# Kernel optimization log

Hardware: AMD Instinct MI355X
Metric: run time of the kernel (lower is better)

## Reference

```python
import jax, jax.numpy as jnp
import numpy as np
from math import sqrt

NUM_HEADS = 16
NUM_KV_HEADS = 4
ROPE_BASE = 10000.0


def setup_inputs() -> dict:
    key = jax.random.key(0)
    ks = jax.random.split(key, 9)
    B, S, E = 4, 2048, 2048
    KV_DIM = NUM_KV_HEADS * (E // NUM_HEADS)  # 512
    s = 0.02
    return {
        "x": jax.random.normal(ks[0], (B, S, E), jnp.float32),
        "wq": jax.random.normal(ks[1], (E, E), jnp.float32) * s,
        "bq": jnp.zeros((E,), jnp.float32),
        "wk": jax.random.normal(ks[2], (KV_DIM, E), jnp.float32) * s,
        "bk": jnp.zeros((KV_DIM,), jnp.float32),
        "wv": jax.random.normal(ks[3], (KV_DIM, E), jnp.float32) * s,
        "bv": jnp.zeros((KV_DIM,), jnp.float32),
        "wo": jax.random.normal(ks[4], (E, E), jnp.float32) * s,
        "bo": jnp.zeros((E,), jnp.float32),
    }


def _rope_cos_sin(seq_len, head_dim, dtype):
    inv_freq = 1.0 / (ROPE_BASE ** (jnp.arange(0, head_dim, 2, dtype=jnp.float32) / head_dim))
    pos = jnp.arange(seq_len, dtype=jnp.float32)
    freqs = pos[:, None] * inv_freq[None, :]            # [S, D/2]
    emb = jnp.concatenate([freqs, freqs], axis=-1)      # [S, D]
    return jnp.cos(emb).astype(dtype), jnp.sin(emb).astype(dtype)


def _apply_rope(t, cos, sin):
    # t: [B, H, S, D]; cos/sin: [S, D]
    d2 = t.shape[-1] // 2
    rot = jnp.concatenate([-t[..., d2:], t[..., :d2]], axis=-1)
    return t * cos[None, None, :, :] + rot * sin[None, None, :, :]


def reference(x, wq, bq, wk, bk, wv, bv, wo, bo):
    B, S, E = x.shape
    H, KV = NUM_HEADS, NUM_KV_HEADS
    D = E // H
    G = H // KV

    q = (x @ wq.T + bq).reshape(B, S, H, D).transpose(0, 2, 1, 3)   # [B,H,S,D]
    k = (x @ wk.T + bk).reshape(B, S, KV, D).transpose(0, 2, 1, 3)  # [B,KV,S,D]
    v = (x @ wv.T + bv).reshape(B, S, KV, D).transpose(0, 2, 1, 3)

    cos, sin = _rope_cos_sin(S, D, x.dtype)
    q = _apply_rope(q, cos, sin)
    k = _apply_rope(k, cos, sin)

    # GQA: expand each kv head group_size times (contiguous repeat)
    k = jnp.repeat(k, G, axis=1)  # [B,H,S,D]
    v = jnp.repeat(v, G, axis=1)

    scores = jnp.einsum("bhqd,bhkd->bhqk", q, k)
    causal = jnp.triu(jnp.ones((S, S), dtype=bool), k=1)
    scores = jnp.where(causal[None, None, :, :], -jnp.inf, scores)
    attn = jax.nn.softmax(scores / sqrt(D), axis=-1)
    out = jnp.einsum("bhqk,bhkd->bhqd", attn, v)        # [B,H,S,D]
    out = out.transpose(0, 2, 1, 3).reshape(B, S, E)
    return out @ wo.T + bo
```

## Files before the change

kernel.cpp:

```cpp
#include <hip/hip_runtime.h>
#include <stdint.h>
#include <math.h>

typedef __attribute__((ext_vector_type(8))) short s16x8;
typedef __attribute__((ext_vector_type(4))) short s16x4;
typedef __attribute__((ext_vector_type(4))) float f32x4;

#define NEGH (-1.0e30f)

__device__ __forceinline__ short f2bf(float f) {
  union { float f; unsigned int i; } c; c.f = f;
  unsigned int lsb = (c.i >> 16) & 1u;
  c.i += 0x7fffu + lsb;
  return (short)(c.i >> 16);
}
__device__ __forceinline__ float bf2f(short u) {
  union { unsigned int i; float f; } c;
  c.i = ((unsigned int)(unsigned short)u) << 16;
  return c.f;
}

#define GLOAD_LDS16(gp, lp)                                                  \
  __builtin_amdgcn_global_load_lds(                                          \
      (__attribute__((address_space(1))) void*)(void*)(gp),                  \
      (__attribute__((address_space(3))) void*)(lp), 16, 0, 0)

__global__ __launch_bounds__(256) void cvt_kernel(const float* __restrict__ in,
                                                  short* __restrict__ out)
{
  const size_t i = ((size_t)blockIdx.x * 256 + threadIdx.x) * 4;
  const float4 v = *(const float4*)(in + i);
  s16x4 o = { f2bf(v.x), f2bf(v.y), f2bf(v.z), f2bf(v.w) };
  *(s16x4*)(out + i) = o;
}

__global__ __launch_bounds__(256) void gemm_bt(
    const short* __restrict__ A, const short* __restrict__ W,
    const float* __restrict__ bias, const float* __restrict__ bias2,
    void* __restrict__ C, void* __restrict__ C2,
    int M, int N, int K, int omode)
{
  __shared__ __align__(16) short As[128 * 64];
  __shared__ __align__(16) short Bs[128 * 64];

  const int t = threadIdx.x;
  const int l = t & 63;
  const int w = t >> 6;
  const int lane16 = l & 15;
  const int quad = l >> 4;
  const int wm = w >> 1, wn = w & 1;

  int bx = blockIdx.x, by = blockIdx.y;
  if (gridDim.x == 8 && gridDim.y == 64) {
    const int lid = blockIdx.x + 8 * blockIdx.y;
    const int xcd = lid & 7, idx = lid >> 3;
    by = xcd * 8 + (idx >> 3);
    bx = idx & 7;
  }
  const int mb0 = by * 128;
  const int nb0 = bx * 128;

  const f32x4 zero = {0.f, 0.f, 0.f, 0.f};
  f32x4 acc[4][4];
#pragma unroll
  for (int i = 0; i < 4; ++i)
#pragma unroll
    for (int j = 0; j < 4; ++j) acc[i][j] = zero;

  const int sr = t >> 3;
  const int sp = t & 7;
  const short* Ag = A + (size_t)(mb0 + sr) * K + sp * 8;
  const short* Wg = W + (size_t)(nb0 + sr) * K + sp * 8;
  short* Al = As + t * 8;
  short* Bl = Bs + t * 8;

  const int nkt = K >> 6;
  for (int kt = 0; kt < nkt; ++kt) {
    __syncthreads();
    const int kof = kt * 64;
#pragma unroll
    for (int it = 0; it < 4; ++it) {
      GLOAD_LDS16(Ag + kof + (size_t)(it * 32) * K, Al + it * 2048);
      GLOAD_LDS16(Wg + kof + (size_t)(it * 32) * K, Bl + it * 2048);
    }
    __syncthreads();
#pragma unroll
    for (int kk = 0; kk < 2; ++kk) {
      s16x8 af[4], bf[4];
#pragma unroll
      for (int mi = 0; mi < 4; ++mi)
        af[mi] = *(const s16x8*)&As[(wm * 64 + mi * 16 + lane16) * 64 +
                                    kk * 32 + quad * 8];
#pragma unroll
      for (int ni = 0; ni < 4; ++ni)
        bf[ni] = *(const s16x8*)&Bs[(wn * 64 + ni * 16 + lane16) * 64 +
                                    kk * 32 + quad * 8];
#pragma unroll
      for (int mi = 0; mi < 4; ++mi)
#pragma unroll
        for (int ni = 0; ni < 4; ++ni)
          acc[mi][ni] = __builtin_amdgcn_mfma_f32_16x16x32_bf16(
              af[mi], bf[ni], acc[mi][ni], 0, 0, 0);
    }
  }

#pragma unroll
  for (int ni = 0; ni < 4; ++ni) {
    const int n = nb0 + wn * 64 + ni * 16 + lane16;
    const float bvx = (omode == 3 && n >= 512) ? bias2[n - 512] : bias[n];
#pragma unroll
    for (int mi = 0; mi < 4; ++mi) {
      const int m0 = mb0 + wm * 64 + mi * 16 + quad * 4;
#pragma unroll
      for (int r = 0; r < 4; ++r) {
        const int m = m0 + r;
        const float v = acc[mi][ni][r] + bvx;
        if (omode == 0) {
          ((short*)C)[(size_t)m * N + n] = f2bf(v);
        } else if (omode == 1) {
          ((float*)C)[(size_t)m * N + n] = v;
        } else {
          if (n < 512) ((short*)C)[(size_t)m * 512 + n] = f2bf(v);
          else         ((short*)C2)[(size_t)m * 512 + (n - 512)] = f2bf(v);
        }
      }
    }
  }
}

__global__ __launch_bounds__(512, 2) void gemm256_bt(
    const short* __restrict__ A, const short* __restrict__ W,
    const float* __restrict__ bias, void* __restrict__ C,
    int M, int N, int K, int omode)
{
  __shared__ __align__(16) short Asm[2 * 16384];
  __shared__ __align__(16) short Bsm[2 * 16384];

  const int t = threadIdx.x;
  const int l = t & 63;
  const int w = t >> 6;
  const int lane16 = l & 15;
  const int quad = l >> 4;
  const int wm = w >> 2;
  const int wn = w & 3;

  int bx = blockIdx.x, by = blockIdx.y;
  if (gridDim.x == 8 && gridDim.y == 32) {
    const int bid = blockIdx.y * 8 + blockIdx.x;
    const int xcd = bid & 7, idx = bid >> 3;
    const int xc = xcd & 3, yc = xcd >> 2;
    bx = xc * 2 + (idx & 1);
    by = yc * 16 + (idx >> 1);
  }
  const int mb0 = by * 256;
  const int nb0 = bx * 256;

  const f32x4 zero = {0.f, 0.f, 0.f, 0.f};
  f32x4 acc[8][4];
#pragma unroll
  for (int i = 0; i < 8; ++i)
#pragma unroll
    for (int j = 0; j < 4; ++j) acc[i][j] = zero;

  const int srow = t >> 2;
  const int scs = (t & 3) ^ ((t >> 3) & 3);
  const short* Ag = A + (size_t)(mb0 + srow) * K + scs * 8;
  const short* Wg = W + (size_t)(nb0 + srow) * K + scs * 8;
  const size_t rstep = (size_t)128 * K;

#define STAGE_A(b, kt, kh)                                                    \
  do {                                                                        \
    const size_t ko_ = (size_t)(kt) * 64 + (kh) * 32;                         \
    GLOAD_LDS16(Ag + ko_,         Asm + (b) * 16384 + (kh) * 8192 + t * 8);   \
    GLOAD_LDS16(Ag + ko_ + rstep, Asm + (b) * 16384 + (kh) * 8192 + 4096 + t * 8); \
  } while (0)
#define STAGE_B(b, kt, kh)                                                    \
  do {                                                                        \
    const size_t ko_ = (size_t)(kt) * 64 + (kh) * 32;                         \
    GLOAD_LDS16(Wg + ko_,         Bsm + (b) * 16384 + (kh) * 8192 + t * 8);   \
    GLOAD_LDS16(Wg + ko_ + rstep, Bsm + (b) * 16384 + (kh) * 8192 + 4096 + t * 8); \
  } while (0)

  s16x8 bfr[4];

#define DO_PHASE(BUF, KK, MG, READB, STAGE_STMT, DO_VM)                       \
  {                                                                           \
    const short* Abase = Asm + (BUF) * 16384 + (KK) * 8192;                   \
    const short* Bbase = Bsm + (BUF) * 16384 + (KK) * 8192;                   \
    if (READB) {                                                              \
      _Pragma("unroll")                                                       \
      for (int ni = 0; ni < 4; ++ni) {                                        \
        const int nr = wn * 64 + ni * 16 + lane16;                            \
        bfr[ni] = *(const s16x8*)(Bbase + nr * 32 +                           \
                                  ((quad ^ ((nr >> 1) & 3)) << 3));           \
      }                                                                       \
    }                                                                         \
    s16x8 afr[4];                                                             \
    _Pragma("unroll")                                                         \
    for (int mi2 = 0; mi2 < 4; ++mi2) {                                       \
      const int mr = wm * 128 + (MG) * 64 + mi2 * 16 + lane16;                \
      afr[mi2] = *(const s16x8*)(Abase + mr * 32 +                            \
                                 ((quad ^ ((mr >> 1) & 3)) << 3));            \
    }                                                                         \
    STAGE_STMT;                                                               \
    __builtin_amdgcn_s_barrier();                                             \
    asm volatile("s_waitcnt lgkmcnt(0)" ::: "memory");                        \
    __builtin_amdgcn_sched_barrier(0);                                        \
    __builtin_amdgcn_s_setprio(1);                                            \
    _Pragma("unroll")                                                         \
    for (int mi2 = 0; mi2 < 4; ++mi2)                                         \
      _Pragma("unroll")                                                       \
      for (int ni = 0; ni < 4; ++ni)                                          \
        acc[(MG) * 4 + mi2][ni] = __builtin_amdgcn_mfma_f32_16x16x32_bf16(    \
            afr[mi2], bfr[ni], acc[(MG) * 4 + mi2][ni], 0, 0, 0);             \
    __builtin_amdgcn_s_setprio(0);                                            \
    if (DO_VM) {                                                              \
      asm volatile("s_waitcnt vmcnt(10)" ::: "memory");                       \
      __builtin_amdgcn_sched_barrier(0);                                      \
    }                                                                         \
    __builtin_amdgcn_s_barrier();                                             \
  }

  const int NT = K >> 6;

  STAGE_B(0, 0, 0); STAGE_A(0, 0, 0); STAGE_B(0, 0, 1); STAGE_A(0, 0, 1);
  STAGE_B(1, 1, 0); STAGE_A(1, 1, 0); STAGE_B(1, 1, 1);
  asm volatile("s_waitcnt vmcnt(10)" ::: "memory");
  __builtin_amdgcn_sched_barrier(0);
  __builtin_amdgcn_s_barrier();

  for (int i2 = 0; i2 < NT; i2 += 2) {
    const int tp1 = (i2 + 1 < NT) ? i2 + 1 : NT - 1;
    const int tp2 = (i2 + 2 < NT) ? i2 + 2 : NT - 1;
    const int tp3 = (i2 + 3 < NT) ? i2 + 3 : NT - 1;
    DO_PHASE(0, 0, 0, true,  STAGE_A(1, tp1, 1), false)
    DO_PHASE(0, 0, 1, false, STAGE_B(0, tp2, 0), true)
    DO_PHASE(0, 1, 0, true,  STAGE_A(0, tp2, 0), false)
    DO_PHASE(0, 1, 1, false, STAGE_B(0, tp2, 1), true)
    DO_PHASE(1, 0, 0, true,  STAGE_A(0, tp2, 1), false)
    DO_PHASE(1, 0, 1, false, STAGE_B(1, tp3, 0), true)
    DO_PHASE(1, 1, 0, true,  STAGE_A(1, tp3, 0), false)
    DO_PHASE(1, 1, 1, false, STAGE_B(1, tp3, 1), true)
  }

#pragma unroll
  for (int ni = 0; ni < 4; ++ni) {
    const int n = nb0 + wn * 64 + ni * 16 + lane16;
    const float bv = bias[n];
#pragma unroll
    for (int mi = 0; mi < 8; ++mi) {
      const int m0 = mb0 + wm * 128 + mi * 16 + quad * 4;
#pragma unroll
      for (int r = 0; r < 4; ++r) {
        const float v = acc[mi][ni][r] + bv;
        if (omode == 0) ((short*)C)[(size_t)(m0 + r) * N + n] = f2bf(v);
        else            ((float*)C)[(size_t)(m0 + r) * N + n] = v;
      }
    }
  }
#undef DO_PHASE
#undef STAGE_A
#undef STAGE_B
}

__global__ __launch_bounds__(256) void rope_tab_kernel(float2* __restrict__ tab)
{
  const int i = blockIdx.x * 256 + threadIdx.x;
  const int pos = i >> 6, d = i & 63;
  const float fr = (float)pos * exp2f((float)d * -0.20762050593048584f);
  float sn, cs;
  sincosf(fr, &sn, &cs);
  tab[i] = make_float2(cs, sn);
}

__global__ __launch_bounds__(256) void rope_kernel(short* __restrict__ buf,
                                                   int lognh,
                                                   const float2* __restrict__ tab)
{
  const int idx = blockIdx.x * 256 + threadIdx.x;
  const int d = idx & 63;
  const int rest = idx >> 6;
  const int row = rest >> lognh;
  const int pos = row & 2047;
  const float2 cssn = tab[(pos << 6) | d];
  const float cs = cssn.x, sn = cssn.y;
  const size_t base = (size_t)rest * 128 + d;
  const float lo = bf2f(buf[base]);
  const float hi = bf2f(buf[base + 64]);
  buf[base]      = f2bf(lo * cs - hi * sn);
  buf[base + 64] = f2bf(hi * cs + lo * sn);
}

__global__ __launch_bounds__(256) void trans_kernel(const short* __restrict__ in,
                                                    short* __restrict__ out)
{
  __shared__ short T[64 * 72];
  const int t = threadIdx.x;
  const int ms = blockIdx.x * 64;
  const int ns = blockIdx.y * 64;
  const int b = ms >> 11;
  const int sl = ms & 2047;
  const int r = t >> 3, sg = t & 7;
#pragma unroll
  for (int j = 0; j < 2; ++j) {
    const uint4 v = *(const uint4*)(in + (size_t)(ms + r + 32 * j) * 512 + ns + sg * 8);
    *(uint4*)&T[(r + 32 * j) * 72 + sg * 8] = v;
  }
  __syncthreads();
#pragma unroll
  for (int j = 0; j < 2; ++j) {
    const int nr = r + 32 * j;
    s16x8 v;
#pragma unroll
    for (int i = 0; i < 8; ++i) v[i] = T[(sg * 8 + i) * 72 + nr];
    *(s16x8*)(out + ((size_t)(b * 512 + ns + nr)) * 2048 + sl + sg * 8) = v;
  }
}

__global__ __launch_bounds__(512, 4) void attn_kernel(
    const short* __restrict__ qg, const short* __restrict__ kg,
    const short* __restrict__ vtg, short* __restrict__ og)
{
  __shared__ __align__(16) short Ksm[64 * 128];
  __shared__ __align__(16) short Vsm[128 * 64];
  __shared__ __align__(16) short Psm[128 * 64];

  const int t = threadIdx.x;
  const int l = t & 63;
  const int w = t >> 6;
  const int lane16 = l & 15;
  const int quad = l >> 4;

  const int lid = blockIdx.x + 8 * (blockIdx.y + 16 * blockIdx.z);
  const int xcd = lid & 7, idx = lid >> 3;
  const int g = xcd * 2 + (idx >> 5);
  const int wv_ = idx & 31;
  const int b = g >> 2, kv = g & 3;
  const int h = kv * 4 + (wv_ >> 3);
  const int jb = wv_ & 7;

  const int krow = t >> 4, kseg = t & 15;
  const int vrow = t >> 3, vseg = t & 7;
  const int kswz = (kseg ^ (krow & 7)) * 8;
  const int vswz = (vseg ^ (vrow & 7)) * 8;

  const short* kbaseptr = kg + ((size_t)(b * 2048)) * 512 + kv * 128;
  const short* vbaseptr = vtg + ((size_t)(b * 512 + kv * 128)) * 2048;

  const float SC = 0.08838834764831845f * 1.4426950408889634f;
  const f32x4 zero = {0.f, 0.f, 0.f, 0.f};
  const int swz = (lane16 & 7) << 3;

  uint4 kr0, kr1, vr0, vr1;
#define LOADT(KB)                                                             \
  do {                                                                        \
    kr0 = *(const uint4*)(kbaseptr + (size_t)((KB) + krow) * 512 + kseg * 8); \
    kr1 = *(const uint4*)(kbaseptr + (size_t)((KB) + 32 + krow) * 512 + kseg * 8); \
    vr0 = *(const uint4*)(vbaseptr + (size_t)(vrow) * 2048 + (KB) + vseg * 8);     \
    vr1 = *(const uint4*)(vbaseptr + (size_t)(64 + vrow) * 2048 + (KB) + vseg * 8);\
  } while (0)
#define WRITET()                                                              \
  do {                                                                        \
    *(uint4*)&Ksm[krow * 128 + kswz] = kr0;                                   \
    *(uint4*)&Ksm[(32 + krow) * 128 + kswz] = kr1;                            \
    *(uint4*)&Vsm[vrow * 64 + vswz] = vr0;                                    \
    *(uint4*)&Vsm[(64 + vrow) * 64 + vswz] = vr1;                             \
  } while (0)

  for (int sp2 = 0; sp2 < 2; ++sp2) {
    const int jj = sp2 ? (15 - jb) : jb;
    const int qb0 = jj * 128;
    const int qw0 = qb0 + w * 16;
    const int qmaxw = qw0 + 15;
    const int ntl = 2 * jj + 2;

    s16x8 qf[4];
    {
      const short* qrow =
          qg + ((size_t)(b * 2048 + qw0 + lane16)) * 2048 + h * 128 + quad * 8;
#pragma unroll
      for (int kk = 0; kk < 4; ++kk) qf[kk] = *(const s16x8*)(qrow + kk * 32);
    }

    f32x4 o[8];
#pragma unroll
    for (int i = 0; i < 8; ++i) o[i] = zero;
    float m_i = NEGH, l_i = 0.f;

    LOADT(0);
    WRITET();

    for (int tl = 0; tl < ntl; ++tl) {
      __syncthreads();
      const int kbase = tl * 64;
      if (tl + 1 < ntl) LOADT((tl + 1) * 64);

      if (kbase <= qmaxw) {
        f32x4 st[4];
#pragma unroll
        for (int mt = 0; mt < 4; ++mt) st[mt] = zero;
        __builtin_amdgcn_s_setprio(1);
#pragma unroll
        for (int mt = 0; mt < 4; ++mt) {
          const int rb = (mt * 16 + lane16) * 128;
#pragma unroll
          for (int kk = 0; kk < 4; ++kk) {
            const s16x8 a = *(const s16x8*)&Ksm[rb + ((kk * 32 + quad * 8) ^ swz)];
            st[mt] = __builtin_amdgcn_mfma_f32_16x16x32_bf16(a, qf[kk], st[mt], 0, 0, 0);
          }
        }
        __builtin_amdgcn_s_setprio(0);

        const bool maskt = (kbase + 63 > qw0);
        const int qabs = qw0 + lane16;
        float tl_ = NEGH;
        if (maskt) {
#pragma unroll
          for (int mt = 0; mt < 4; ++mt)
#pragma unroll
            for (int r = 0; r < 4; ++r) {
              float xx = st[mt][r];
              if ((kbase + mt * 16 + quad * 4 + r) > qabs) xx = NEGH;
              st[mt][r] = xx;
              tl_ = fmaxf(tl_, xx);
            }
        } else {
#pragma unroll
          for (int mt = 0; mt < 4; ++mt)
#pragma unroll
            for (int r = 0; r < 4; ++r) tl_ = fmaxf(tl_, st[mt][r]);
        }
        tl_ = fmaxf(tl_, __shfl_xor(tl_, 16));
        tl_ = fmaxf(tl_, __shfl_xor(tl_, 32));
        const float mnew = fmaxf(m_i, tl_);
        if (!__all(tl_ <= m_i)) {
          const float alpha = exp2f((m_i - mnew) * SC);
          l_i *= alpha;
#pragma unroll
          for (int r = 0; r < 4; ++r) {
            const float ar = __shfl(alpha, quad * 4 + r);
#pragma unroll
            for (int ntd = 0; ntd < 8; ++ntd) o[ntd][r] *= ar;
          }
        }
        m_i = mnew;
        const float mS = mnew * SC;
        float rs = 0.f;
#pragma unroll
        for (int mt = 0; mt < 4; ++mt) {
          const float p0 = exp2f(fmaf(st[mt][0], SC, -mS));
          const float p1 = exp2f(fmaf(st[mt][1], SC, -mS));
          const float p2 = exp2f(fmaf(st[mt][2], SC, -mS));
          const float p3 = exp2f(fmaf(st[mt][3], SC, -mS));
          rs += (p0 + p1) + (p2 + p3);
          uint2 pk2;
          asm("v_cvt_pk_bf16_f32 %0, %1, %2" : "=v"(pk2.x) : "v"(p0), "v"(p1));
          asm("v_cvt_pk_bf16_f32 %0, %1, %2" : "=v"(pk2.y) : "v"(p2), "v"(p3));
          *(uint2*)&Psm[(w * 16 + lane16) * 64 + ((mt * 16 + quad * 4) ^ swz)] = pk2;
        }
        rs += __shfl_xor(rs, 16);
        rs += __shfl_xor(rs, 32);
        l_i += rs;

        const int prb = (w * 16 + lane16) * 64;
        __builtin_amdgcn_s_setprio(1);
#pragma unroll
        for (int kk = 0; kk < 2; ++kk) {
          const s16x8 pf = *(const s16x8*)&Psm[prb + ((kk * 32 + quad * 8) ^ swz)];
#pragma unroll
          for (int ntd = 0; ntd < 8; ++ntd) {
            const s16x8 vf =
                *(const s16x8*)&Vsm[(ntd * 16 + lane16) * 64 + ((kk * 32 + quad * 8) ^ swz)];
            o[ntd] = __builtin_amdgcn_mfma_f32_16x16x32_bf16(pf, vf, o[ntd], 0, 0, 0);
          }
        }
        __builtin_amdgcn_s_setprio(0);
      }

      __syncthreads();
      if (tl + 1 < ntl) WRITET();
    }

#pragma unroll
    for (int r = 0; r < 4; ++r) {
      const float lr = __shfl(l_i, quad * 4 + r);
      const float inv = 1.f / lr;
      const size_t base =
          ((size_t)(b * 2048 + qw0 + quad * 4 + r)) * 2048 + h * 128 + lane16;
#pragma unroll
      for (int ntd = 0; ntd < 8; ++ntd) og[base + ntd * 16] = f2bf(o[ntd][r] * inv);
    }
  }
#undef LOADT
#undef WRITET
}

extern "C" void kernel_launch(void* const* d_in, const int* in_sizes, int n_in,
                              void* d_out, int out_size, void* d_ws,
                              size_t ws_size, hipStream_t stream)
{
  const float* x  = (const float*)d_in[0];
  const float* wq = (const float*)d_in[1];
  const float* bq = (const float*)d_in[2];
  const float* wk = (const float*)d_in[3];
  const float* bk = (const float*)d_in[4];
  const float* wv = (const float*)d_in[5];
  const float* bv = (const float*)d_in[6];
  const float* wo = (const float*)d_in[7];
  const float* bo = (const float*)d_in[8];
  float* out = (float*)d_out;

  char* ws = (char*)d_ws;
  short* xb  = (short*)ws;
  short* wqb = (short*)(ws + (32ull << 20));
  short* wkb = (short*)(ws + (40ull << 20));
  short* wvb = (short*)(ws + (42ull << 20));
  short* qws = (short*)(ws + (44ull << 20));
  float2* tab = (float2*)(ws + (76ull << 20));
  short* wob = xb;
  short* kws = (short*)d_out;
  short* vtw = (short*)((char*)d_out + (8ull << 20));
  short* vtmp = (short*)((char*)d_out + (16ull << 20));

  const dim3 blk(256);
  cvt_kernel<<<16384, blk, 0, stream>>>(x,  xb);
  cvt_kernel<<<4096,  blk, 0, stream>>>(wq, wqb);
  cvt_kernel<<<1024,  blk, 0, stream>>>(wk, wkb);
  cvt_kernel<<<1024,  blk, 0, stream>>>(wv, wvb);
  rope_tab_kernel<<<512, blk, 0, stream>>>(tab);
  gemm256_bt<<<dim3(8, 32), dim3(512), 0, stream>>>(xb, wqb, bq, qws, 8192, 2048, 2048, 0);
  gemm_bt<<<dim3(8, 64), blk, 0, stream>>>(xb, wkb, bk, bv, kws, vtmp, 8192, 1024, 2048, 3);
  trans_kernel<<<dim3(128, 8), blk, 0, stream>>>(vtmp, vtw);
  rope_kernel<<<32768, blk, 0, stream>>>(qws, 4, tab);
  rope_kernel<<<8192,  blk, 0, stream>>>(kws, 2, tab);
  cvt_kernel<<<4096, blk, 0, stream>>>(wo, wob);
  attn_kernel<<<dim3(8, 16, 4), dim3(512), 0, stream>>>(qws, kws, vtw, qws);
  gemm256_bt<<<dim3(8, 32), dim3(512), 0, stream>>>(qws, wob, bo, out, 8192, 2048, 2048, 1);
}
```

Before: 531.1 us.

## Fuse Q RoPE into attention and double-buffer K/V shared memory tiles

Drops the separate RoPE pass over Q and instead rotates the Q fragments in registers inside the attention kernel, reading the cos/sin table. K/V shared-memory tiles are double-buffered, so the next tile is written into the alternate buffer before a single barrier per iteration instead of two. This removes one full read/write pass over Q and one barrier per tile. In exchange it doubles K/V LDS use (about 80KB per block), which may cut occupancy below the launch-bounds target.

```diff
diff --git a/kernel.cpp b/kernel.cpp
--- a/kernel.cpp
+++ b/kernel.cpp
@@ -319,10 +319,11 @@
 
 __global__ __launch_bounds__(512, 4) void attn_kernel(
     const short* __restrict__ qg, const short* __restrict__ kg,
-    const short* __restrict__ vtg, short* __restrict__ og)
-{
-  __shared__ __align__(16) short Ksm[64 * 128];
-  __shared__ __align__(16) short Vsm[128 * 64];
+    const short* __restrict__ vtg, short* __restrict__ og,
+    const float2* __restrict__ tab)
+{
+  __shared__ __align__(16) short Ksm[2 * 64 * 128];
+  __shared__ __align__(16) short Vsm[2 * 128 * 64];
   __shared__ __align__(16) short Psm[128 * 64];
 
   const int t = threadIdx.x;
@@ -359,12 +360,12 @@
     vr0 = *(const uint4*)(vbaseptr + (size_t)(vrow) * 2048 + (KB) + vseg * 8);     \
     vr1 = *(const uint4*)(vbaseptr + (size_t)(64 + vrow) * 2048 + (KB) + vseg * 8);\
   } while (0)
-#define WRITET()                                                              \
+#define WRITET(c)                                                             \
   do {                                                                        \
-    *(uint4*)&Ksm[krow * 128 + kswz] = kr0;                                   \
-    *(uint4*)&Ksm[(32 + krow) * 128 + kswz] = kr1;                            \
-    *(uint4*)&Vsm[vrow * 64 + vswz] = vr0;                                    \
-    *(uint4*)&Vsm[(64 + vrow) * 64 + vswz] = vr1;                             \
+    *(uint4*)&Ksm[(c) * 8192 + krow * 128 + kswz] = kr0;                      \
+    *(uint4*)&Ksm[(c) * 8192 + (32 + krow) * 128 + kswz] = kr1;               \
+    *(uint4*)&Vsm[(c) * 8192 + vrow * 64 + vswz] = vr0;                       \
+    *(uint4*)&Vsm[(c) * 8192 + (64 + vrow) * 64 + vswz] = vr1;                \
   } while (0)
 
   for (int sp2 = 0; sp2 < 2; ++sp2) {
@@ -378,8 +379,32 @@
     {
       const short* qrow =
           qg + ((size_t)(b * 2048 + qw0 + lane16)) * 2048 + h * 128 + quad * 8;
-#pragma unroll
-      for (int kk = 0; kk < 4; ++kk) qf[kk] = *(const s16x8*)(qrow + kk * 32);
+      s16x8 qr[4];
+#pragma unroll
+      for (int kk = 0; kk < 4; ++kk) qr[kk] = *(const s16x8*)(qrow + kk * 32);
+      const float2* tb = tab + (((size_t)(qw0 + lane16)) << 6) + quad * 8;
+#pragma unroll
+      for (int kk = 0; kk < 2; ++kk) {
+        float lo[8], hi[8];
+#pragma unroll
+        for (int j = 0; j < 8; ++j) {
+          const float2 cs2 = tb[kk * 32 + j];
+          const float l0 = bf2f(qr[kk][j]);
+          const float h0 = bf2f(qr[kk + 2][j]);
+          lo[j] = l0 * cs2.x - h0 * cs2.y;
+          hi[j] = h0 * cs2.x + l0 * cs2.y;
+        }
+        union { unsigned int u[4]; s16x8 v; } plo, phi;
+#pragma unroll
+        for (int j = 0; j < 4; ++j) {
+          asm("v_cvt_pk_bf16_f32 %0, %1, %2"
+              : "=v"(plo.u[j]) : "v"(lo[2 * j]), "v"(lo[2 * j + 1]));
+          asm("v_cvt_pk_bf16_f32 %0, %1, %2"
+              : "=v"(phi.u[j]) : "v"(hi[2 * j]), "v"(hi[2 * j + 1]));
+        }
+        qf[kk] = plo.v;
+        qf[kk + 2] = phi.v;
+      }
     }
 
     f32x4 o[8];
@@ -388,14 +413,17 @@
     float m_i = NEGH, l_i = 0.f;
 
     LOADT(0);
-    WRITET();
+    WRITET(0);
+    __syncthreads();
+    int cur = 0;
 
     for (int tl = 0; tl < ntl; ++tl) {
-      __syncthreads();
       const int kbase = tl * 64;
       if (tl + 1 < ntl) LOADT((tl + 1) * 64);
 
       if (kbase <= qmaxw) {
+        const short* Kb = Ksm + cur * 8192;
+        const short* Vb = Vsm + cur * 8192;
         f32x4 st[4];
 #pragma unroll
         for (int mt = 0; mt < 4; ++mt) st[mt] = zero;
@@ -405,7 +433,7 @@
           const int rb = (mt * 16 + lane16) * 128;
 #pragma unroll
           for (int kk = 0; kk < 4; ++kk) {
-            const s16x8 a = *(const s16x8*)&Ksm[rb + ((kk * 32 + quad * 8) ^ swz)];
+            const s16x8 a = *(const s16x8*)&Kb[rb + ((kk * 32 + quad * 8) ^ swz)];
             st[mt] = __builtin_amdgcn_mfma_f32_16x16x32_bf16(a, qf[kk], st[mt], 0, 0, 0);
           }
         }
@@ -470,15 +498,16 @@
 #pragma unroll
           for (int ntd = 0; ntd < 8; ++ntd) {
             const s16x8 vf =
-                *(const s16x8*)&Vsm[(ntd * 16 + lane16) * 64 + ((kk * 32 + quad * 8) ^ swz)];
+                *(const s16x8*)&Vb[(ntd * 16 + lane16) * 64 + ((kk * 32 + quad * 8) ^ swz)];
             o[ntd] = __builtin_amdgcn_mfma_f32_16x16x32_bf16(pf, vf, o[ntd], 0, 0, 0);
           }
         }
         __builtin_amdgcn_s_setprio(0);
       }
 
+      if (tl + 1 < ntl) WRITET(cur ^ 1);
       __syncthreads();
-      if (tl + 1 < ntl) WRITET();
+      cur ^= 1;
     }
 
 #pragma unroll
@@ -531,9 +560,8 @@
   gemm256_bt<<<dim3(8, 32), dim3(512), 0, stream>>>(xb, wqb, bq, qws, 8192, 2048, 2048, 0);
   gemm_bt<<<dim3(8, 64), blk, 0, stream>>>(xb, wkb, bk, bv, kws, vtmp, 8192, 1024, 2048, 3);
   trans_kernel<<<dim3(128, 8), blk, 0, stream>>>(vtmp, vtw);
-  rope_kernel<<<32768, blk, 0, stream>>>(qws, 4, tab);
-  rope_kernel<<<8192,  blk, 0, stream>>>(kws, 2, tab);
+  rope_kernel<<<8192, blk, 0, stream>>>(kws, 2, tab);
   cvt_kernel<<<4096, blk, 0, stream>>>(wo, wob);
-  attn_kernel<<<dim3(8, 16, 4), dim3(512), 0, stream>>>(qws, kws, vtw, qws);
+  attn_kernel<<<dim3(8, 16, 4), dim3(512), 0, stream>>>(qws, kws, vtw, qws, tab);
   gemm256_bt<<<dim3(8, 32), dim3(512), 0, stream>>>(qws, wob, bo, out, 8192, 2048, 2048, 1);
 }
```

Result: faster. 504.9 us (-4.9%).
